# Optimization experiments

Hardware: AMD Instinct MI355X
Metric: run time of the kernel (lower is better)

Reference implementation:

```python
import jax, jax.numpy as jnp
import numpy as np
import math

H = 12   # num_attention_heads
DH = 64  # attention_head_size
HID = H * DH  # 768


def setup_inputs() -> dict:
    key = jax.random.key(0)
    ks = jax.random.split(key, 16)
    B, S = 2, 128
    inp = {
        'hidden_states': jax.random.normal(ks[0], (B, S, HID), jnp.float32),
        'attention_mask': jnp.zeros((B, 1, 1, S), jnp.float32),
        'inference_path': jax.random.normal(ks[1], (B, S, S, HID), jnp.float32),
        'span_mask': jax.random.uniform(ks[2], (B, 1, S, S), jnp.float32),
    }
    sc = 1.0 / math.sqrt(HID)
    # weights stored as [in, out]; y = x @ W + b
    inp['Wq'] = jax.random.normal(ks[3], (HID, HID), jnp.float32) * sc
    inp['bq'] = jnp.zeros((HID,), jnp.float32)
    inp['Wk'] = jax.random.normal(ks[4], (HID, HID), jnp.float32) * sc
    inp['bk'] = jnp.zeros((HID,), jnp.float32)
    inp['Wv'] = jax.random.normal(ks[5], (HID, HID), jnp.float32) * sc
    inp['bv'] = jnp.zeros((HID,), jnp.float32)
    inp['Wpv'] = jax.random.normal(ks[6], (HID, DH), jnp.float32) * sc
    inp['bpv'] = jnp.zeros((DH,), jnp.float32)
    inp['Wip'] = jax.random.normal(ks[7], (HID, 2 * HID), jnp.float32) * sc
    inp['Wmlp'] = jax.random.normal(ks[8], (HID + DH, HID), jnp.float32) * sc
    inp['bmlp'] = jnp.zeros((HID,), jnp.float32)
    return inp


def reference(hidden_states, attention_mask, inference_path, span_mask,
              Wq, bq, Wk, bk, Wv, bv, Wpv, bpv, Wip, Wmlp, bmlp):
    B, S, _ = hidden_states.shape
    # projections
    q = (hidden_states @ Wq + bq).reshape(B, S, H, DH).transpose(0, 2, 1, 3)  # [B,H,S,Dh]
    k = (hidden_states @ Wk + bk).reshape(B, S, H, DH).transpose(0, 2, 1, 3)
    v = (hidden_states @ Wv + bv).reshape(B, S, H, DH).transpose(0, 2, 1, 3)
    # parse value path: [B,1,S,Dh]
    pv = (hidden_states @ Wpv + bpv).reshape(B, S, 1, DH).transpose(0, 2, 1, 3)
    parse_ctx = jnp.matmul(span_mask, pv)              # [B,1,S,Dh]
    parse_ctx = parse_ctx.transpose(0, 2, 1, 3)        # [B,S,1,Dh]
    # relative inference-path bias: raw view (matches torch .view semantics)
    ip = inference_path @ Wip                           # [B,S,S,2*HID]
    ra, rb = jnp.split(ip, 2, axis=-1)                  # each [B,S,S,HID]
    ra = ra.reshape(B, H, S, S, DH)
    rb = rb.reshape(B, H, S, S, DH)
    qe = q[:, :, :, None, :] + ra                       # [B,H,S,S,Dh]
    ke = k[:, :, None, :, :] + rb                       # [B,H,S,S,Dh]
    scores = jnp.einsum('bhqkd,bhqkd->bhqk', qe, ke)
    scores = scores / math.sqrt(DH) + attention_mask
    probs = jax.nn.softmax(scores, axis=-1)             # dropout is identity in eval
    ctx = jnp.matmul(probs, v)                          # [B,H,S,Dh]
    ctx = ctx.transpose(0, 2, 1, 3)                     # [B,S,H,Dh]
    ctx = jnp.concatenate([ctx, parse_ctx], axis=-2)    # [B,S,H+1,Dh]
    ctx = ctx.reshape(B, S, HID + DH)
    return ctx @ Wmlp + bmlp                            # [B,S,HID]
```

## Files before the change

kernel.cpp:

```cpp
#include <hip/hip_runtime.h>
#include <hip/hip_bf16.h>


typedef __attribute__((ext_vector_type(8))) __bf16 bf16x8;
typedef __attribute__((ext_vector_type(16))) float f32x16;
typedef __attribute__((ext_vector_type(4))) float f32x4;

#define QKV_OFF   0u
#define ARENA_OFF 2424832u
#define SC_OFF    4784128u
#define CTX_OFF   6356992u

__global__ __launch_bounds__(256)
void prep_proj_kernel(const float* __restrict__ Wip, __bf16* __restrict__ arena,
                      const float* __restrict__ hs,
                      const float* __restrict__ Wq, const float* __restrict__ bq,
                      const float* __restrict__ Wk, const float* __restrict__ bk,
                      const float* __restrict__ Wv, const float* __restrict__ bv,
                      const float* __restrict__ Wpv, const float* __restrict__ bpv,
                      float* __restrict__ qkv) {
  if (blockIdx.x < 576) {
    const int l = threadIdx.x & 63;
    const int f = blockIdx.x * 4 + (threadIdx.x >> 6);
    const int n32 = f / 48, k16 = f - n32 * 48;
    const float* src = Wip + (size_t)(k16 * 16 + (l >> 5) * 8) * 1536 + n32 * 32 + (l & 31);
    union { __bf16 h[8]; uint4 u; } pk;
#pragma unroll
    for (int j = 0; j < 8; j++) pk.h[j] = (__bf16)src[(size_t)j * 1536];
    ((uint4*)arena)[(size_t)f * 64 + l] = pk.u;
    return;
  }
  const int pblk = blockIdx.x - 576;
  const int n0 = (pblk % 74) * 32;
  const int m0 = (pblk / 74) * 128 + (threadIdx.x >> 6) * 32;
  const float* W; const float* bias; int noff, ldw;
  if (n0 < 768)       { W = Wq;  bias = bq;  noff = n0;        ldw = 768; }
  else if (n0 < 1536) { W = Wk;  bias = bk;  noff = n0 - 768;  ldw = 768; }
  else if (n0 < 2304) { W = Wv;  bias = bv;  noff = n0 - 1536; ldw = 768; }
  else                { W = Wpv; bias = bpv; noff = n0 - 2304; ldw = 64;  }
  const int l = threadIdx.x & 63;
  const int rsel = l & 31, ksel = l >> 5;
  f32x16 acc;
#pragma unroll
  for (int z = 0; z < 16; z++) acc[z] = 0.f;

#pragma unroll 4
  for (int k16 = 0; k16 < 48; k16++) {
    const float* ap = hs + (size_t)(m0 + rsel) * 768 + k16 * 16 + ksel * 8;
    float4 a0 = *(const float4*)ap;
    float4 a1 = *(const float4*)(ap + 4);
    union { __bf16 h[8]; bf16x8 v; } pa;
    pa.h[0] = (__bf16)a0.x; pa.h[1] = (__bf16)a0.y; pa.h[2] = (__bf16)a0.z; pa.h[3] = (__bf16)a0.w;
    pa.h[4] = (__bf16)a1.x; pa.h[5] = (__bf16)a1.y; pa.h[6] = (__bf16)a1.z; pa.h[7] = (__bf16)a1.w;
    const float* bp = W + (size_t)(k16 * 16 + ksel * 8) * ldw + noff + rsel;
    union { __bf16 h[8]; bf16x8 v; } pb;
#pragma unroll
    for (int j = 0; j < 8; j++) pb.h[j] = (__bf16)bp[(size_t)j * ldw];
    acc = __builtin_amdgcn_mfma_f32_32x32x16_bf16(pa.v, pb.v, acc, 0, 0, 0);
  }
#pragma unroll
  for (int reg = 0; reg < 16; reg++) {
    int row = (reg & 3) + ((reg >> 2) << 3) + (ksel << 2);
    qkv[(size_t)(m0 + row) * 2368 + n0 + rsel] = acc[reg] + bias[noff + rsel];
  }
}

extern __shared__ char smem_raw[];

__global__ __launch_bounds__(512, 2)
void score_kernel(const float* __restrict__ infp,
                  const __bf16* __restrict__ arena,
                  const float* __restrict__ qkv,
                  const float* __restrict__ mask,
                  float* __restrict__ probs) {
  char* Abase = smem_raw;
  float* lds_sc = (float*)(smem_raw + 99840);
  const int tid = threadIdx.x;
  const int lane = tid & 63;
  const int ml = lane & 31;
  const int kh = lane >> 5;
  const int wv = tid >> 6;
  const int wc = wv & 3;
  const int wd = wv >> 2;
  const int blk = blockIdx.x;
  const int b = blk >> 8;
  const int r0 = (blk & 255) << 6;

  for (int z = tid; z < 768; z += 512) lds_sc[z] = 0.f;

  const uint4* BA = (const uint4*)arena;
  const uint4* bptr  = BA + (size_t)((2 * wc + wd) * 48) * 64 + lane;
  const uint4* bptr2 = bptr + 73728;
  int kpn = 0;
  uint4 B0[8], B1[8], B2[8];
  bf16x8 Af[8];
  f32x16 acc_ra[2], acc_rb[2];

  auto loadB = [&](uint4* dst) {
#pragma unroll
    for (int ks = 0; ks < 4; ks++) {
      dst[ks * 2]     = bptr[ks * 64];
      dst[ks * 2 + 1] = bptr2[ks * 64];
    }
    if (kpn == 11) { bptr += 21760; bptr2 += 21760; kpn = 0; }
    else           { bptr += 256;   bptr2 += 256;   kpn++;  }
  };

  loadB(B0);
  loadB(B1);

  {
    const f32x4* A4 = (const f32x4*)(infp + (size_t)(b * 16384 + r0) * 768);
#pragma unroll
    for (int p = 0; p < 12; p++) {
      int idx = p * 512 + tid;
      int m = (int)(((unsigned)idx * 10923u) >> 20);
      int g = idx - m * 96;
      f32x4 v0 = __builtin_nontemporal_load(A4 + m * 192 + g * 2);
      f32x4 v1 = __builtin_nontemporal_load(A4 + m * 192 + g * 2 + 1);
      union { __bf16 h[8]; uint4 u; } pk;
      pk.h[0] = (__bf16)v0[0]; pk.h[1] = (__bf16)v0[1];
      pk.h[2] = (__bf16)v0[2]; pk.h[3] = (__bf16)v0[3];
      pk.h[4] = (__bf16)v1[0]; pk.h[5] = (__bf16)v1[1];
      pk.h[6] = (__bf16)v1[2]; pk.h[7] = (__bf16)v1[3];
      int F = (m >> 5) * 48 + (g >> 1);
      int slot = (m & 31) + ((g & 1) << 5);
      *(uint4*)(Abase + ((F * 65 + slot) << 4)) = pk.u;
    }
  }
  __syncthreads();

  const size_t lane_off = (size_t)(lane << 4);
  auto loadA = [&](int kcc) {
    const char* ab = Abase + lane_off + kcc * 4160;
#pragma unroll
    for (int mt = 0; mt < 2; mt++)
#pragma unroll
      for (int ks = 0; ks < 4; ks++)
        Af[mt * 4 + ks] = *(const bf16x8*)(ab + mt * 49920 + ks * 1040);
  };
  auto mfma_step = [&](const uint4* Bb) {
#pragma unroll
    for (int ks = 0; ks < 4; ks++) {
      bf16x8 bra = __builtin_bit_cast(bf16x8, Bb[ks * 2]);
      bf16x8 brb = __builtin_bit_cast(bf16x8, Bb[ks * 2 + 1]);
#pragma unroll
      for (int mt = 0; mt < 2; mt++) {
        acc_ra[mt] = __builtin_amdgcn_mfma_f32_32x32x16_bf16(Af[mt * 4 + ks], bra, acc_ra[mt], 0, 0, 0);
        acc_rb[mt] = __builtin_amdgcn_mfma_f32_32x32x16_bf16(Af[mt * 4 + ks], brb, acc_rb[mt], 0, 0, 0);
      }
    }
  };
  auto epilogue = [&](int c) {
    int d = wd * 32 + ml;
#pragma unroll
    for (int mt = 0; mt < 2; mt++) {
      float qv[16], kv[16];
#pragma unroll
      for (int reg = 0; reg < 16; reg++) {
        int row = mt * 32 + (reg & 3) + ((reg >> 2) << 3) + (kh << 2);
        int t = 12 * (r0 + row) + c;
        int hh = t >> 14;
        int ii = (t >> 7) & 127;
        int jj = t & 127;
        qv[reg] = qkv[(size_t)((b << 7) + ii) * 2368 + (hh << 6) + d];
        kv[reg] = qkv[(size_t)((b << 7) + jj) * 2368 + 768 + (hh << 6) + d];
      }
#pragma unroll
      for (int reg = 0; reg < 16; reg++) {
        int row = mt * 32 + (reg & 3) + ((reg >> 2) << 3) + (kh << 2);
        float p = (qv[reg] + acc_ra[mt][reg]) * (kv[reg] + acc_rb[mt][reg]);
        p += __shfl_xor(p, 16);
        p += __shfl_xor(p, 8);
        p += __shfl_xor(p, 4);
        p += __shfl_xor(p, 2);
        p += __shfl_xor(p, 1);
        if (ml == 0) atomicAdd(&lds_sc[row * 12 + c], p);
      }
    }
#pragma unroll
    for (int mt = 0; mt < 2; mt++)
#pragma unroll
      for (int z = 0; z < 16; z++) { acc_ra[mt][z] = 0.f; acc_rb[mt][z] = 0.f; }
  };

#pragma unroll
  for (int mt = 0; mt < 2; mt++)
#pragma unroll
    for (int z = 0; z < 16; z++) { acc_ra[mt][z] = 0.f; acc_rb[mt][z] = 0.f; }

  int kcc = 0, cc = wc;
#pragma unroll 1
  for (int it = 0; it < 12; it++) {
    {
      loadB(B2);
      loadA(kcc);
      mfma_step(B0);
      if (kcc == 11) { epilogue(cc); kcc = 0; cc += 4; } else kcc++;
    }
    {
      if (it < 11) loadB(B0);
      loadA(kcc);
      mfma_step(B1);
      if (kcc == 11) { epilogue(cc); kcc = 0; cc += 4; } else kcc++;
    }
    {
      if (it < 11) loadB(B1);
      loadA(kcc);
      mfma_step(B2);
      if (kcc == 11) { epilogue(cc); kcc = 0; cc += 4; } else kcc++;
    }
  }

  __syncthreads();
  if (wv < 6) {
    const int z0 = wv << 7;
    float s0 = lds_sc[z0 + lane] * 0.125f + mask[b * 128 + lane];
    float s1 = lds_sc[z0 + lane + 64] * 0.125f + mask[b * 128 + lane + 64];
    float mx = fmaxf(s0, s1);
#pragma unroll
    for (int o = 32; o; o >>= 1) mx = fmaxf(mx, __shfl_xor(mx, o));
    float e0 = __expf(s0 - mx), e1 = __expf(s1 - mx);
    float sm = e0 + e1;
#pragma unroll
    for (int o = 32; o; o >>= 1) sm += __shfl_xor(sm, o);
    float inv = 1.f / sm;
    const int t0 = 12 * r0 + z0;
    const int hh = t0 >> 14;
    const int ii = (t0 >> 7) & 127;
    float* dst = probs + (size_t)((b * 12 + hh) * 128 + ii) * 128;
    dst[lane] = e0 * inv;
    dst[lane + 64] = e1 * inv;
  }
}

__global__ __launch_bounds__(256)
void attn_kernel(const float* __restrict__ probs, const float* __restrict__ qkv,
                 const float* __restrict__ span, float* __restrict__ ctx) {
  const int i = blockIdx.x;
  const int b = blockIdx.y;
  const int tid = threadIdx.x;
  const int l = tid & 63;
  const int wvi = tid >> 6;
  __shared__ float w[13][132];
  for (int r = wvi; r < 13; r += 4) {
    const float* sp = (r < 12)
        ? probs + (size_t)((b * 12 + r) * 128 + i) * 128
        : span + (size_t)(b * 128 + i) * 128;
    w[r][l] = sp[l];
    w[r][l + 64] = sp[l + 64];
  }
  __syncthreads();
  if (tid < 208) {
    const int h = tid >> 4;
    const int d4 = (tid & 15) << 2;
    const float* vp = qkv + (size_t)(b * 128) * 2368 + (h < 12 ? 1536 + h * 64 : 2304) + d4;
    f32x4 acc = {0.f, 0.f, 0.f, 0.f};
#pragma unroll 8
    for (int j = 0; j < 128; j++) {
      f32x4 v = *(const f32x4*)(vp + (size_t)j * 2368);
      float ww = w[h][j];
      acc[0] += ww * v[0]; acc[1] += ww * v[1];
      acc[2] += ww * v[2]; acc[3] += ww * v[3];
    }
    *(f32x4*)(ctx + (size_t)(b * 128 + i) * 832 + (h < 12 ? h * 64 : 768) + d4) = acc;
  }
}

__global__ __launch_bounds__(256)
void out_kernel(const float* __restrict__ ctxb, const float* __restrict__ Wmlp,
                const float* __restrict__ bmlp, float* __restrict__ out) {
  const int n0 = blockIdx.x * 32;
  const int m0 = blockIdx.y * 128 + (threadIdx.x >> 6) * 32;
  const int l = threadIdx.x & 63;
  const int rsel = l & 31, ksel = l >> 5;
  f32x16 acc;
#pragma unroll
  for (int z = 0; z < 16; z++) acc[z] = 0.f;

#pragma unroll 4
  for (int k16 = 0; k16 < 52; k16++) {
    const float* ap = ctxb + (size_t)(m0 + rsel) * 832 + k16 * 16 + ksel * 8;
    float4 a0 = *(const float4*)ap;
    float4 a1 = *(const float4*)(ap + 4);
    union { __bf16 h[8]; bf16x8 v; } pa;
    pa.h[0] = (__bf16)a0.x; pa.h[1] = (__bf16)a0.y; pa.h[2] = (__bf16)a0.z; pa.h[3] = (__bf16)a0.w;
    pa.h[4] = (__bf16)a1.x; pa.h[5] = (__bf16)a1.y; pa.h[6] = (__bf16)a1.z; pa.h[7] = (__bf16)a1.w;
    const float* bp = Wmlp + (size_t)(k16 * 16 + ksel * 8) * 768 + n0 + rsel;
    union { __bf16 h[8]; bf16x8 v; } pb;
#pragma unroll
    for (int j = 0; j < 8; j++) pb.h[j] = (__bf16)bp[(size_t)j * 768];
    acc = __builtin_amdgcn_mfma_f32_32x32x16_bf16(pa.v, pb.v, acc, 0, 0, 0);
  }
#pragma unroll
  for (int reg = 0; reg < 16; reg++) {
    int row = (reg & 3) + ((reg >> 2) << 3) + (ksel << 2);
    out[(size_t)(m0 + row) * 768 + n0 + rsel] = acc[reg] + bmlp[n0 + rsel];
  }
}

extern "C" void kernel_launch(void* const* d_in, const int* in_sizes, int n_in,
                              void* d_out, int out_size, void* d_ws, size_t ws_size,
                              hipStream_t stream) {
  const float* hs   = (const float*)d_in[0];
  const float* mask = (const float*)d_in[1];
  const float* infp = (const float*)d_in[2];
  const float* span = (const float*)d_in[3];
  const float* Wq   = (const float*)d_in[4];
  const float* bq   = (const float*)d_in[5];
  const float* Wk   = (const float*)d_in[6];
  const float* bk   = (const float*)d_in[7];
  const float* Wv   = (const float*)d_in[8];
  const float* bv   = (const float*)d_in[9];
  const float* Wpv  = (const float*)d_in[10];
  const float* bpv  = (const float*)d_in[11];
  const float* Wip  = (const float*)d_in[12];
  const float* Wmlp = (const float*)d_in[13];
  const float* bmlp = (const float*)d_in[14];
  float* out = (float*)d_out;

  char* ws = (char*)d_ws;
  float*  qkv    = (float*)(ws + QKV_OFF);
  __bf16* arena  = (__bf16*)(ws + ARENA_OFF);
  float*  probs  = (float*)(ws + SC_OFF);
  float*  ctx    = (float*)(ws + CTX_OFF);

  prep_proj_kernel<<<dim3(724), 256, 0, stream>>>(Wip, arena, hs,
      Wq, bq, Wk, bk, Wv, bv, Wpv, bpv, qkv);
  score_kernel<<<dim3(512), 512, 102912, stream>>>(infp, arena, qkv, mask, probs);
  attn_kernel<<<dim3(128, 2), 256, 0, stream>>>(probs, qkv, span, ctx);
  out_kernel<<<dim3(24, 2), 256, 0, stream>>>(ctx, Wmlp, bmlp, out);
}
```

Measured before the change: 329.7 us.

## Split score kernel ra/rb GEMMs across two wave groups with LDS handoff

```diff
diff --git a/kernel.cpp b/kernel.cpp
--- a/kernel.cpp
+++ b/kernel.cpp
@@ -67,7 +67,7 @@
 
 extern __shared__ char smem_raw[];
 
-__global__ __launch_bounds__(512, 2)
+__global__ __launch_bounds__(1024, 2)
 void score_kernel(const float* __restrict__ infp,
                   const __bf16* __restrict__ arena,
                   const float* __restrict__ qkv,
@@ -75,45 +75,42 @@
                   float* __restrict__ probs) {
   char* Abase = smem_raw;
   float* lds_sc = (float*)(smem_raw + 99840);
+  float* hand   = (float*)(smem_raw + 102912);
   const int tid = threadIdx.x;
   const int lane = tid & 63;
   const int ml = lane & 31;
   const int kh = lane >> 5;
   const int wv = tid >> 6;
-  const int wc = wv & 3;
-  const int wd = wv >> 2;
+  const int wv8 = wv & 7;
+  const int wr = wv >> 3;
+  const int wc = wv8 & 3;
+  const int wd = wv8 >> 2;
   const int blk = blockIdx.x;
   const int b = blk >> 8;
   const int r0 = (blk & 255) << 6;
 
-  for (int z = tid; z < 768; z += 512) lds_sc[z] = 0.f;
-
-  const uint4* BA = (const uint4*)arena;
-  const uint4* bptr  = BA + (size_t)((2 * wc + wd) * 48) * 64 + lane;
-  const uint4* bptr2 = bptr + 73728;
+  for (int z = tid; z < 768; z += 1024) lds_sc[z] = 0.f;
+
+  const uint4* bptr = (const uint4*)arena + (size_t)((2 * wc + wd) * 48) * 64
+                      + (size_t)wr * 73728 + lane;
   int kpn = 0;
-  uint4 B0[8], B1[8], B2[8];
+  bf16x8 B0[4], B1[4];
   bf16x8 Af[8];
-  f32x16 acc_ra[2], acc_rb[2];
-
-  auto loadB = [&](uint4* dst) {
-#pragma unroll
-    for (int ks = 0; ks < 4; ks++) {
-      dst[ks * 2]     = bptr[ks * 64];
-      dst[ks * 2 + 1] = bptr2[ks * 64];
-    }
-    if (kpn == 11) { bptr += 21760; bptr2 += 21760; kpn = 0; }
-    else           { bptr += 256;   bptr2 += 256;   kpn++;  }
+  f32x16 acc[2];
+
+  auto loadB = [&](bf16x8* dst) {
+#pragma unroll
+    for (int ks = 0; ks < 4; ks++) dst[ks] = *(const bf16x8*)(bptr + ks * 64);
+    if (kpn == 11) { bptr += 21760; kpn = 0; } else { bptr += 256; kpn++; }
   };
 
   loadB(B0);
-  loadB(B1);
 
   {
     const f32x4* A4 = (const f32x4*)(infp + (size_t)(b * 16384 + r0) * 768);
 #pragma unroll
-    for (int p = 0; p < 12; p++) {
-      int idx = p * 512 + tid;
+    for (int p = 0; p < 6; p++) {
+      int idx = p * 1024 + tid;
       int m = (int)(((unsigned)idx * 10923u) >> 20);
       int g = idx - m * 96;
       f32x4 v0 = __builtin_nontemporal_load(A4 + m * 192 + g * 2);
@@ -139,76 +136,82 @@
       for (int ks = 0; ks < 4; ks++)
         Af[mt * 4 + ks] = *(const bf16x8*)(ab + mt * 49920 + ks * 1040);
   };
-  auto mfma_step = [&](const uint4* Bb) {
-#pragma unroll
-    for (int ks = 0; ks < 4; ks++) {
-      bf16x8 bra = __builtin_bit_cast(bf16x8, Bb[ks * 2]);
-      bf16x8 brb = __builtin_bit_cast(bf16x8, Bb[ks * 2 + 1]);
-#pragma unroll
-      for (int mt = 0; mt < 2; mt++) {
-        acc_ra[mt] = __builtin_amdgcn_mfma_f32_32x32x16_bf16(Af[mt * 4 + ks], bra, acc_ra[mt], 0, 0, 0);
-        acc_rb[mt] = __builtin_amdgcn_mfma_f32_32x32x16_bf16(Af[mt * 4 + ks], brb, acc_rb[mt], 0, 0, 0);
-      }
-    }
+  auto mfma_step = [&](const bf16x8* Bb) {
+#pragma unroll
+    for (int ks = 0; ks < 4; ks++)
+#pragma unroll
+      for (int mt = 0; mt < 2; mt++)
+        acc[mt] = __builtin_amdgcn_mfma_f32_32x32x16_bf16(Af[mt * 4 + ks], Bb[ks], acc[mt], 0, 0, 0);
   };
   auto epilogue = [&](int c) {
-    int d = wd * 32 + ml;
+    const int d = wd * 32 + ml;
 #pragma unroll
     for (int mt = 0; mt < 2; mt++) {
-      float qv[16], kv[16];
-#pragma unroll
-      for (int reg = 0; reg < 16; reg++) {
-        int row = mt * 32 + (reg & 3) + ((reg >> 2) << 3) + (kh << 2);
-        int t = 12 * (r0 + row) + c;
-        int hh = t >> 14;
-        int ii = (t >> 7) & 127;
-        int jj = t & 127;
-        qv[reg] = qkv[(size_t)((b << 7) + ii) * 2368 + (hh << 6) + d];
-        kv[reg] = qkv[(size_t)((b << 7) + jj) * 2368 + 768 + (hh << 6) + d];
+      if (wr == 0) {
+#pragma unroll
+        for (int q = 0; q < 4; q++) {
+          f32x4 w4;
+          w4[0] = acc[mt][q * 4 + 0]; w4[1] = acc[mt][q * 4 + 1];
+          w4[2] = acc[mt][q * 4 + 2]; w4[3] = acc[mt][q * 4 + 3];
+          *(f32x4*)(hand + (wv8 * 4 + q) * 256 + lane * 4) = w4;
+        }
       }
-#pragma unroll
-      for (int reg = 0; reg < 16; reg++) {
-        int row = mt * 32 + (reg & 3) + ((reg >> 2) << 3) + (kh << 2);
-        float p = (qv[reg] + acc_ra[mt][reg]) * (kv[reg] + acc_rb[mt][reg]);
-        p += __shfl_xor(p, 16);
-        p += __shfl_xor(p, 8);
-        p += __shfl_xor(p, 4);
-        p += __shfl_xor(p, 2);
-        p += __shfl_xor(p, 1);
-        if (ml == 0) atomicAdd(&lds_sc[row * 12 + c], p);
+      __syncthreads();
+      if (wr == 1) {
+#pragma unroll
+        for (int q = 0; q < 4; q++) {
+          f32x4 ra4 = *(const f32x4*)(hand + (wv8 * 4 + q) * 256 + lane * 4);
+          float qv[4], kv[4];
+#pragma unroll
+          for (int j = 0; j < 4; j++) {
+            int row = mt * 32 + j + q * 8 + (kh << 2);
+            int t = 12 * (r0 + row) + c;
+            int hh = t >> 14;
+            int ii = (t >> 7) & 127;
+            int jj = t & 127;
+            qv[j] = qkv[(size_t)((b << 7) + ii) * 2368 + (hh << 6) + d];
+            kv[j] = qkv[(size_t)((b << 7) + jj) * 2368 + 768 + (hh << 6) + d];
+          }
+#pragma unroll
+          for (int j = 0; j < 4; j++) {
+            int row = mt * 32 + j + q * 8 + (kh << 2);
+            float p = (qv[j] + ra4[j]) * (kv[j] + acc[mt][q * 4 + j]);
+            p += __shfl_xor(p, 16);
+            p += __shfl_xor(p, 8);
+            p += __shfl_xor(p, 4);
+            p += __shfl_xor(p, 2);
+            p += __shfl_xor(p, 1);
+            if (ml == 0) atomicAdd(&lds_sc[row * 12 + c], p);
+          }
+        }
       }
+      __syncthreads();
     }
 #pragma unroll
     for (int mt = 0; mt < 2; mt++)
 #pragma unroll
-      for (int z = 0; z < 16; z++) { acc_ra[mt][z] = 0.f; acc_rb[mt][z] = 0.f; }
+      for (int z = 0; z < 16; z++) acc[mt][z] = 0.f;
   };
 
 #pragma unroll
   for (int mt = 0; mt < 2; mt++)
 #pragma unroll
-    for (int z = 0; z < 16; z++) { acc_ra[mt][z] = 0.f; acc_rb[mt][z] = 0.f; }
-
-  int kcc = 0, cc = wc;
+    for (int z = 0; z < 16; z++) acc[mt][z] = 0.f;
+
+  int kc = 0, c = wc;
 #pragma unroll 1
-  for (int it = 0; it < 12; it++) {
+  for (int it = 0; it < 18; it++) {
     {
-      loadB(B2);
-      loadA(kcc);
+      loadB(B1);
+      loadA(kc);
       mfma_step(B0);
-      if (kcc == 11) { epilogue(cc); kcc = 0; cc += 4; } else kcc++;
+      if (kc == 11) { epilogue(c); kc = 0; c += 4; } else kc++;
     }
     {
-      if (it < 11) loadB(B0);
-      loadA(kcc);
+      if (it < 17) loadB(B0);
+      loadA(kc);
       mfma_step(B1);
-      if (kcc == 11) { epilogue(cc); kcc = 0; cc += 4; } else kcc++;
-    }
-    {
-      if (it < 11) loadB(B1);
-      loadA(kcc);
-      mfma_step(B2);
-      if (kcc == 11) { epilogue(cc); kcc = 0; cc += 4; } else kcc++;
+      if (kc == 11) { epilogue(c); kc = 0; c += 4; } else kc++;
     }
   }
 
@@ -327,7 +330,7 @@
 
   prep_proj_kernel<<<dim3(724), 256, 0, stream>>>(Wip, arena, hs,
       Wq, bq, Wk, bk, Wv, bv, Wpv, bpv, qkv);
-  score_kernel<<<dim3(512), 512, 102912, stream>>>(infp, arena, qkv, mask, probs);
+  score_kernel<<<dim3(512), 1024, 135680, stream>>>(infp, arena, qkv, mask, probs);
   attn_kernel<<<dim3(128, 2), 256, 0, stream>>>(probs, qkv, span, ctx);
   out_kernel<<<dim3(24, 2), 256, 0, stream>>>(ctx, Wmlp, bmlp, out);
 }
```

Measured after the change: 350.6 us. +6.4%, slower.
